# Optimization experiments

Measured on AMD Instinct MI355X. Metric: run time of the kernel, lower is better.

The kernel has to match this reference:

```python
import jax, jax.numpy as jnp
import numpy as np

B, C, H, W = 32, 3, 128, 128
HID, NP, P, E, NH = 64, 64, 16, 768, 4
MAX_SCALE = 0.3


def conv3x3(x, w, b):
    y = jax.lax.conv_general_dilated(x, w, (1, 1), 'SAME', dimension_numbers=('NCHW', 'OIHW', 'NCHW'))
    return y + b[None, :, None, None]


def mha(t, qkv_w, qkv_b, out_w, out_b):
    # t: (B, T, E) -> standard multi-head self-attention (eval: no dropout)
    b, T, e = t.shape
    dh = e // NH
    qkv = t @ qkv_w.T + qkv_b
    q, k, v = jnp.split(qkv, 3, axis=-1)
    sh = lambda z: z.reshape(b, T, NH, dh).transpose(0, 2, 1, 3)
    q, k, v = sh(q), sh(k), sh(v)
    a = jax.nn.softmax(jnp.einsum('bhqd,bhkd->bhqk', q, k) * np.float32(1.0 / np.sqrt(dh)), axis=-1)
    o = jnp.einsum('bhqk,bhkd->bhqd', a, v).transpose(0, 2, 1, 3).reshape(b, T, e)
    return o @ out_w.T + out_b


def conv_self_attn(x, in_w, in_b, qkv_w, qkv_b, out_w, out_b, proj_w, proj_b):
    # channels are tokens; project spatial dim H*W -> E, attend, project back
    b, c, h, w = x.shape
    t = x.reshape(b, c, h * w) @ in_w.T + in_b
    t = mha(t, qkv_w, qkv_b, out_w, out_b)
    y = t @ proj_w.T + proj_b
    return y.reshape(b, c, h, w)


def maxpool2(x):
    return jax.lax.reduce_window(x, -jnp.inf, jax.lax.max, (1, 1, 2, 2), (1, 1, 2, 2), 'VALID')


def grid_sample_bilinear(img, gx, gy):
    # img: (B,C,H,W); gx,gy: (B,NP,P,P) normalized coords; align_corners=False, zeros padding
    b, c, h, w = img.shape
    xs = ((gx + 1.0) * w - 1.0) * 0.5
    ys = ((gy + 1.0) * h - 1.0) * 0.5
    x0f = jnp.floor(xs); y0f = jnp.floor(ys)
    wx = xs - x0f; wy = ys - y0f
    x0 = x0f.astype(jnp.int32); x1 = x0 + 1
    y0 = y0f.astype(jnp.int32); y1 = y0 + 1
    flat = img.reshape(b, c, h * w)

    def gather(yi, xi):
        valid = (xi >= 0) & (xi < w) & (yi >= 0) & (yi < h)
        idx = jnp.clip(yi, 0, h - 1) * w + jnp.clip(xi, 0, w - 1)
        vals = jax.vmap(lambda f, i: f[:, i])(flat, idx)  # (B,C,NP,P,P)
        return vals * valid[:, None].astype(img.dtype)

    v00 = gather(y0, x0); v01 = gather(y0, x1)
    v10 = gather(y1, x0); v11 = gather(y1, x1)
    wxb = wx[:, None]; wyb = wy[:, None]  # (B,1,NP,P,P)
    out = (v00 * (1 - wxb) * (1 - wyb) + v01 * wxb * (1 - wyb)
           + v10 * (1 - wxb) * wyb + v11 * wxb * wyb)
    return out.transpose(0, 2, 1, 3, 4).reshape(b * NP, c, P, P)


def setup_inputs() -> dict:
    key = jax.random.key(0)
    ks = jax.random.split(key, 32)
    wgt = lambda k, s: jax.random.normal(k, s, dtype=jnp.float32) * 0.02
    HW1, HW2, HC = H * W, (H // 2) * (W // 2), (H // 2) * (W // 2)
    inp = {}
    inp['x'] = jax.random.normal(ks[0], (B, C, H, W), dtype=jnp.float32)
    inp['conv1_w'] = wgt(ks[1], (HID, C, 3, 3)); inp['conv1_b'] = jnp.zeros((HID,), jnp.float32)
    inp['a1_in_w'] = wgt(ks[2], (E, HW1)); inp['a1_in_b'] = jnp.zeros((E,), jnp.float32)
    inp['a1_qkv_w'] = wgt(ks[3], (3 * E, E)); inp['a1_qkv_b'] = jnp.zeros((3 * E,), jnp.float32)
    inp['a1_out_w'] = wgt(ks[4], (E, E)); inp['a1_out_b'] = jnp.zeros((E,), jnp.float32)
    inp['a1_proj_w'] = wgt(ks[5], (HW1, E)); inp['a1_proj_b'] = jnp.zeros((HW1,), jnp.float32)
    inp['conv2_w'] = wgt(ks[6], (NP, HID, 3, 3)); inp['conv2_b'] = jnp.zeros((NP,), jnp.float32)
    inp['a2_in_w'] = wgt(ks[7], (E, HW2)); inp['a2_in_b'] = jnp.zeros((E,), jnp.float32)
    inp['a2_qkv_w'] = wgt(ks[8], (3 * E, E)); inp['a2_qkv_b'] = jnp.zeros((3 * E,), jnp.float32)
    inp['a2_out_w'] = wgt(ks[9], (E, E)); inp['a2_out_b'] = jnp.zeros((E,), jnp.float32)
    inp['a2_proj_w'] = wgt(ks[10], (HW2, E)); inp['a2_proj_b'] = jnp.zeros((HW2,), jnp.float32)
    inp['fc1_w'] = wgt(ks[11], (HC // 2, HC)); inp['fc1_b'] = jnp.zeros((HC // 2,), jnp.float32)
    inp['fc2_w'] = wgt(ks[12], (4, HC // 2)); inp['fc2_b'] = jnp.zeros((4,), jnp.float32)
    return inp


def reference(x, conv1_w, conv1_b, a1_in_w, a1_in_b, a1_qkv_w, a1_qkv_b, a1_out_w, a1_out_b,
              a1_proj_w, a1_proj_b, conv2_w, conv2_b, a2_in_w, a2_in_b, a2_qkv_w, a2_qkv_b,
              a2_out_w, a2_out_b, a2_proj_w, a2_proj_b, fc1_w, fc1_b, fc2_w, fc2_b):
    b = x.shape[0]
    f = jax.nn.relu(conv3x3(x, conv1_w, conv1_b))
    f = conv_self_attn(f, a1_in_w, a1_in_b, a1_qkv_w, a1_qkv_b, a1_out_w, a1_out_b, a1_proj_w, a1_proj_b)
    f = maxpool2(f)
    f = jax.nn.relu(conv3x3(f, conv2_w, conv2_b))
    f = conv_self_attn(f, a2_in_w, a2_in_b, a2_qkv_w, a2_qkv_b, a2_out_w, a2_out_b, a2_proj_w, a2_proj_b)
    feats = f.reshape(b, NP, -1)
    h1 = jax.nn.relu(feats @ fc1_w.T + fc1_b)
    tp = h1 @ fc2_w.T + fc2_b  # (b, NP, 4)
    translate = jnp.tanh(tp[:, :, :2])
    s = jax.nn.sigmoid(tp[:, :, 2:3]) * MAX_SCALE
    sx = s[:, :, 0]; sy = s[:, :, 0]  # isotropic: repeat
    rot = jnp.tanh(tp[:, :, 3]) * np.float32(np.pi)
    cos = jnp.cos(rot); sin = jnp.sin(rot)
    x_ext = jnp.minimum(sx * jnp.abs(cos) + sy * jnp.abs(sin), 1.0)
    y_ext = jnp.minimum(sx * jnp.abs(sin) + sy * jnp.abs(cos), 1.0)
    translate = translate * (1.0 - jnp.stack([x_ext, y_ext], axis=-1))
    ta = sx * cos; tb_ = -sx * sin; tc = sy * sin; td = sy * cos
    tx = translate[:, :, 0]; ty = translate[:, :, 1]
    base = (2.0 * jnp.arange(P, dtype=jnp.float32) + 1.0) / P - 1.0  # align_corners=False grid
    gx = ta[..., None, None] * base[None, None, None, :] + tb_[..., None, None] * base[None, None, :, None] + tx[..., None, None]
    gy = tc[..., None, None] * base[None, None, None, :] + td[..., None, None] * base[None, None, :, None] + ty[..., None, None]
    patches = grid_sample_bilinear(x, gx, gy)  # (B*NP, C, P, P)
    return (patches, translate)
```

## Files before the change

kernel.cpp:

```cpp
#include <hip/hip_runtime.h>
#include <hip/hip_bf16.h>
#include <math.h>


#define PI_F 3.14159265358979323846f

typedef float f32x4 __attribute__((ext_vector_type(4)));
typedef short short8 __attribute__((ext_vector_type(8)));
typedef unsigned short us4 __attribute__((ext_vector_type(4)));
typedef __hip_bfloat16 bf16;

__device__ __forceinline__ void async16(const void* g, void* l) {
  __builtin_amdgcn_global_load_lds(
      (const __attribute__((address_space(1))) void*)g,
      (__attribute__((address_space(3))) void*)l, 16, 0, 0);
}

template <int MODE>
__global__ __launch_bounds__(256) void gemm_bf16(
    const unsigned short* __restrict__ A, const unsigned short* __restrict__ Bw,
    const float* __restrict__ bias, void* __restrict__ Cout,
    int M, int N, int K, int kchunk) {
  __shared__ unsigned short As[128 * 32];
  __shared__ unsigned short Bs[128 * 32];
  const int tid = threadIdx.x;
  const int bm = blockIdx.y << 7, bn = blockIdx.x << 7;
  const int k0 = blockIdx.z * kchunk;
  const int wave = tid >> 6;
  const int lane = tid & 63;
  const int wm = (wave & 1) << 6, wn = (wave >> 1) << 6;
  const int r0 = tid >> 2;
  const int c0 = (tid & 3) << 3;
  const unsigned short* Ag0 = A + (size_t)(bm + r0) * K + k0 + c0;
  const unsigned short* Ag1 = Ag0 + (size_t)64 * K;
  const unsigned short* Bg0 = Bw + (size_t)(bn + r0) * K + k0 + c0;
  const unsigned short* Bg1 = Bg0 + (size_t)64 * K;
  unsigned short* Al = As + wave * 512;
  unsigned short* Bl = Bs + wave * 512;
  f32x4 acc[4][4] = {};
  const int fr = lane & 15;
  const int fk = (lane >> 4) << 3;
  for (int kt = 0; kt < kchunk; kt += 32) {
    async16(Ag0 + kt, Al);
    async16(Ag1 + kt, Al + 2048);
    async16(Bg0 + kt, Bl);
    async16(Bg1 + kt, Bl + 2048);
    __syncthreads();
    short8 af[4], bf[4];
    #pragma unroll
    for (int i = 0; i < 4; ++i)
      af[i] = *(const short8*)(As + ((wm + i * 16 + fr) << 5) + fk);
    #pragma unroll
    for (int i = 0; i < 4; ++i)
      bf[i] = *(const short8*)(Bs + ((wn + i * 16 + fr) << 5) + fk);
    #pragma unroll
    for (int mi = 0; mi < 4; ++mi)
      #pragma unroll
      for (int ni = 0; ni < 4; ++ni)
        acc[mi][ni] = __builtin_amdgcn_mfma_f32_16x16x32_bf16(af[mi], bf[ni], acc[mi][ni], 0, 0, 0);
    __syncthreads();
  }
  const int cr = (lane >> 4) << 2;
  const int cc = lane & 15;
  if (MODE == 0) {
    float* C = (float*)Cout + (size_t)blockIdx.z * M * N;
    #pragma unroll
    for (int mi = 0; mi < 4; ++mi)
      #pragma unroll
      for (int ni = 0; ni < 4; ++ni) {
        int col = bn + wn + ni * 16 + cc;
        #pragma unroll
        for (int r = 0; r < 4; ++r)
          C[(size_t)(bm + wm + mi * 16 + cr + r) * N + col] = acc[mi][ni][r];
      }
  } else {
    #pragma unroll
    for (int ni = 0; ni < 4; ++ni) {
      int col = bn + wn + ni * 16 + cc;
      float bv = bias[col];
      #pragma unroll
      for (int mi = 0; mi < 4; ++mi)
        #pragma unroll
        for (int r = 0; r < 4; ++r) {
          size_t idx = (size_t)(bm + wm + mi * 16 + cr + r) * N + col;
          float v = acc[mi][ni][r] + bv;
          if (MODE == 1) ((float*)Cout)[idx] = v;
          else ((bf16*)Cout)[idx] = __float2bfloat16(v);
        }
    }
  }
}

__global__ __launch_bounds__(256) void reduce_bias_k(
    const float* __restrict__ part, const float* __restrict__ bias,
    bf16* __restrict__ out, int MN, int N, int S, int relu) {
  int i = blockIdx.x * 256 + threadIdx.x;
  if (i >= MN) return;
  float s = 0.f;
  for (int z = 0; z < S; ++z) s += part[(size_t)z * MN + i];
  s += bias[i % N];
  if (relu) s = fmaxf(s, 0.f);
  out[i] = __float2bfloat16(s);
}

__global__ __launch_bounds__(256) void cvt_bf16_k(
    const float* __restrict__ src, bf16* __restrict__ dst, int n4) {
  int i = blockIdx.x * 256 + threadIdx.x;
  if (i >= n4) return;
  float4 v = ((const float4*)src)[i];
  bf16* d = dst + (size_t)i * 4;
  d[0] = __float2bfloat16(v.x); d[1] = __float2bfloat16(v.y);
  d[2] = __float2bfloat16(v.z); d[3] = __float2bfloat16(v.w);
}

__global__ __launch_bounds__(256) void cvt_wcl_k(
    const float* __restrict__ w, bf16* __restrict__ wcl) {
  int i = blockIdx.x * 256 + threadIdx.x;
  if (i >= 36864) return;
  int ic = i & 63, oc = (i >> 6) & 63, s = i >> 12;
  wcl[i] = __float2bfloat16(w[oc * 576 + ic * 9 + s]);
}

__global__ __launch_bounds__(256) void conv3x3_relu_c3_fast(
    const float* __restrict__ x, const float* __restrict__ w,
    const float* __restrict__ bias, bf16* __restrict__ out) {
  __shared__ float xs[3][4][132];
  __shared__ float wsm[3][9][64];
  const int tid = threadIdx.x;
  const int b = blockIdx.y;
  const int y0 = blockIdx.x * 2;
  const int xg = (tid & 15) * 8;
  const int row = (tid >> 4) & 1;
  const int oc0 = (tid >> 5) * 8;
  for (int i = tid; i < 3 * 4 * 132; i += 256) {
    int c = i % 132;
    int r = (i / 132) % 4;
    int ic = i / (132 * 4);
    int gy = y0 + r - 1;
    int gx = c - 1;
    float v = 0.f;
    if ((unsigned)gy < 128u && (unsigned)gx < 128u)
      v = x[((size_t)(b * 3 + ic) << 14) + gy * 128 + gx];
    xs[ic][r][c] = v;
  }
  for (int i = tid; i < 3 * 9 * 64; i += 256) {
    int oc = i & 63;
    int k = (i >> 6) % 9;
    int ic = i / (64 * 9);
    wsm[ic][k][oc] = w[oc * 27 + ic * 9 + k];
  }
  __syncthreads();
  float acc[8][8] = {};
  #pragma unroll
  for (int ic = 0; ic < 3; ++ic) {
    #pragma unroll
    for (int ky = 0; ky < 3; ++ky) {
      const float* rp = &xs[ic][row + ky][xg];
      float4 r0 = *(const float4*)(rp);
      float4 r1 = *(const float4*)(rp + 4);
      float4 r2 = *(const float4*)(rp + 8);
      float v[10] = {r0.x, r0.y, r0.z, r0.w, r1.x, r1.y, r1.z, r1.w, r2.x, r2.y};
      #pragma unroll
      for (int kx = 0; kx < 3; ++kx) {
        const float* wr = &wsm[ic][ky * 3 + kx][oc0];
        float4 w0 = *(const float4*)(wr);
        float4 w1 = *(const float4*)(wr + 4);
        float wv[8] = {w0.x, w0.y, w0.z, w0.w, w1.x, w1.y, w1.z, w1.w};
        #pragma unroll
        for (int o = 0; o < 8; ++o)
          #pragma unroll
          for (int p = 0; p < 8; ++p)
            acc[o][p] += wv[o] * v[p + kx];
      }
    }
  }
  #pragma unroll
  for (int o = 0; o < 8; ++o) {
    float bo = bias[oc0 + o];
    bf16 vals[8];
    #pragma unroll
    for (int p = 0; p < 8; ++p) vals[p] = __float2bfloat16(fmaxf(acc[o][p] + bo, 0.f));
    bf16* op = out + ((size_t)(b * 64 + oc0 + o) << 14) + (y0 + row) * 128 + xg;
    *(uint4*)op = *(const uint4*)vals;
  }
}

__global__ __launch_bounds__(256) void maxpool_cl(
    const bf16* __restrict__ y1, bf16* __restrict__ xp) {
  int wave = threadIdx.x >> 6;
  int lane = threadIdx.x & 63;
  int cell = blockIdx.x * 4 + wave;
  int b = blockIdx.y;
  int yp = cell / 66, xq = cell % 66;
  bf16* dst = xp + (((size_t)b * 66 + yp) * 66 + xq) * 64 + lane;
  if (yp == 0 || yp == 65 || xq == 0 || xq == 65) {
    *dst = __float2bfloat16(0.f);
    return;
  }
  int py = yp - 1, px = xq - 1;
  const bf16* sp = y1 + ((size_t)(b * 64 + lane) << 14) + (py * 2) * 128 + px * 2;
  float a = __bfloat162float(sp[0]), bq = __bfloat162float(sp[1]);
  float c = __bfloat162float(sp[128]), d = __bfloat162float(sp[129]);
  *dst = __float2bfloat16(fmaxf(fmaxf(a, bq), fmaxf(c, d)));
}

__global__ __launch_bounds__(256) void conv2_mfma(
    const bf16* __restrict__ xp, const bf16* __restrict__ wcl,
    const float* __restrict__ bias, bf16* __restrict__ f3) {
  __shared__ unsigned short As[128 * 32];
  __shared__ unsigned short Bs[64 * 32];
  const int tid = threadIdx.x;
  const int b = blockIdx.y;
  const int y0 = blockIdx.x * 2;
  const int wave = tid >> 6;
  const int lane = tid & 63;
  const int wm = (wave & 1) << 6;
  const int wn = (wave >> 1) << 5;
  const char* xpB = (const char*)(xp + (size_t)b * 66 * 66 * 64);
  const char* wclB = (const char*)wcl;
  const int sr = tid >> 2;
  const int soff = (tid & 3) << 4;
  unsigned short* Al = As + wave * 512;
  unsigned short* Bl = Bs + wave * 512;
  f32x4 acc[4][2] = {};
  const int fr = lane & 15;
  const int fk = (lane >> 4) << 3;
  for (int tap = 0; tap < 9; ++tap) {
    int dy = tap / 3, dx = tap % 3;
    const char* arow0 = xpB + (((y0 + dy) * 66 + dx) << 7);
    const char* brow = wclB + (tap << 13);
    #pragma unroll
    for (int ch = 0; ch < 2; ++ch) {
      int coff = (ch << 6) + soff;
      async16(arow0 + sr * 128 + coff, Al);
      async16(arow0 + 66 * 128 + sr * 128 + coff, Al + 2048);
      async16(brow + sr * 128 + coff, Bl);
      __syncthreads();
      short8 af[4], bf[2];
      #pragma unroll
      for (int i = 0; i < 4; ++i)
        af[i] = *(const short8*)(As + ((wm + i * 16 + fr) << 5) + fk);
      #pragma unroll
      for (int i = 0; i < 2; ++i)
        bf[i] = *(const short8*)(Bs + ((wn + i * 16 + fr) << 5) + fk);
      #pragma unroll
      for (int mi = 0; mi < 4; ++mi)
        #pragma unroll
        for (int ni = 0; ni < 2; ++ni)
          acc[mi][ni] = __builtin_amdgcn_mfma_f32_16x16x32_bf16(af[mi], bf[ni], acc[mi][ni], 0, 0, 0);
      __syncthreads();
    }
  }
  const int cr = (lane >> 4) << 2;
  const int cc = lane & 15;
  #pragma unroll
  for (int ni = 0; ni < 2; ++ni) {
    int oc = wn + ni * 16 + cc;
    float bv = bias[oc];
    #pragma unroll
    for (int mi = 0; mi < 4; ++mi) {
      int pxb = wm + mi * 16 + cr;
      int y = y0 + (pxb >> 6), xb = pxb & 63;
      bf16 vals[4];
      #pragma unroll
      for (int r = 0; r < 4; ++r)
        vals[r] = __float2bfloat16(fmaxf(acc[mi][ni][r] + bv, 0.f));
      bf16* op = f3 + (((size_t)(b * 64 + oc)) << 12) + y * 64 + xb;
      *(us4*)op = *(const us4*)vals;
    }
  }
}

__global__ __launch_bounds__(64) void attn_scores(
    const float* __restrict__ qkv, float* __restrict__ p, float scale) {
  int tq = blockIdx.x, h = blockIdx.y, b = blockIdx.z;
  int lane = threadIdx.x;
  __shared__ float qrow[192];
  const float* qp = qkv + ((size_t)(b * 64 + tq)) * 2304 + h * 192;
  for (int d = lane; d < 192; d += 64) qrow[d] = qp[d];
  __syncthreads();
  const float* kp = qkv + ((size_t)(b * 64 + lane)) * 2304 + 768 + h * 192;
  float s = 0.f;
  for (int d = 0; d < 192; ++d) s += qrow[d] * kp[d];
  s *= scale;
  float m = s;
  for (int off = 32; off; off >>= 1) m = fmaxf(m, __shfl_xor(m, off));
  float e = expf(s - m);
  float sum = e;
  for (int off = 32; off; off >>= 1) sum += __shfl_xor(sum, off);
  p[(((size_t)b * 4 + h) * 64 + tq) * 64 + lane] = e / sum;
}

__global__ __launch_bounds__(256) void attn_o(
    const float* __restrict__ p, const float* __restrict__ qkv, bf16* __restrict__ o) {
  size_t tid = (size_t)blockIdx.x * 256 + threadIdx.x;
  if (tid >= (size_t)32 * 64 * 768) return;
  int e = (int)(tid % 768);
  int tq = (int)((tid / 768) % 64);
  int b = (int)(tid / (768 * 64));
  int h = e / 192;
  const float* pp = p + (((size_t)b * 4 + h) * 64 + tq) * 64;
  const float* vp = qkv + (size_t)b * 64 * 2304 + 1536 + e;
  float acc = 0.f;
  for (int tk = 0; tk < 64; ++tk) acc += pp[tk] * vp[(size_t)tk * 2304];
  o[tid] = __float2bfloat16(acc);
}

__global__ __launch_bounds__(256) void fc2_wave(
    const bf16* __restrict__ A, const float* __restrict__ Bw,
    const float* __restrict__ bias, float* __restrict__ C, int K) {
  int m = blockIdx.x;
  int n = threadIdx.x >> 6;
  int lane = threadIdx.x & 63;
  const bf16* a = A + (size_t)m * K;
  const float* bb = Bw + (size_t)n * K;
  float acc = 0.f;
  for (int k = lane; k < K; k += 64)
    acc += __bfloat162float(a[k]) * bb[k];
  for (int off = 32; off; off >>= 1) acc += __shfl_xor(acc, off);
  if (lane == 0) C[m * 4 + n] = acc + bias[n];
}

__global__ __launch_bounds__(64) void params_k(
    const float* __restrict__ tp, float* __restrict__ par, float* __restrict__ trans_out) {
  int m = blockIdx.x * 64 + threadIdx.x;
  if (m >= 2048) return;
  float t0 = tp[m * 4 + 0], t1 = tp[m * 4 + 1], t2 = tp[m * 4 + 2], t3 = tp[m * 4 + 3];
  float trx = tanhf(t0), tryy = tanhf(t1);
  float s = (1.f / (1.f + expf(-t2))) * 0.3f;
  float rot = tanhf(t3) * PI_F;
  float c = cosf(rot), sn = sinf(rot);
  float x_ext = fminf(s * fabsf(c) + s * fabsf(sn), 1.f);
  float y_ext = fminf(s * fabsf(sn) + s * fabsf(c), 1.f);
  float tx = trx * (1.f - x_ext);
  float ty = tryy * (1.f - y_ext);
  par[m * 8 + 0] = s * c;
  par[m * 8 + 1] = -s * sn;
  par[m * 8 + 2] = s * sn;
  par[m * 8 + 3] = s * c;
  par[m * 8 + 4] = tx;
  par[m * 8 + 5] = ty;
  trans_out[m * 2 + 0] = tx;
  trans_out[m * 2 + 1] = ty;
}

__global__ __launch_bounds__(256) void sample_k(
    const float* __restrict__ x, const float* __restrict__ par, float* __restrict__ out) {
  int tid = blockIdx.x * 256 + threadIdx.x;
  if (tid >= 32 * 64 * 3 * 256) return;
  int pj = tid & 15, pi = (tid >> 4) & 15;
  int c = (tid >> 8) % 3;
  int bp = tid / 768;
  int b = bp >> 6;
  const float* pp = par + bp * 8;
  float ta = pp[0], tb = pp[1], tc = pp[2], td = pp[3], tx = pp[4], ty = pp[5];
  float bj = (2.f * pj + 1.f) / 16.f - 1.f;
  float bi = (2.f * pi + 1.f) / 16.f - 1.f;
  float gx = ta * bj + tb * bi + tx;
  float gy = tc * bj + td * bi + ty;
  float xs = ((gx + 1.f) * 128.f - 1.f) * 0.5f;
  float ys = ((gy + 1.f) * 128.f - 1.f) * 0.5f;
  float x0f = floorf(xs), y0f = floorf(ys);
  float wx = xs - x0f, wy = ys - y0f;
  int x0 = (int)x0f, y0 = (int)y0f, x1 = x0 + 1, y1 = y0 + 1;
  const float* img = x + ((size_t)b * 3 + c) * 16384;
  auto g = [&](int yi, int xi) -> float {
    bool v = (xi >= 0) && (xi < 128) && (yi >= 0) && (yi < 128);
    int yc = yi < 0 ? 0 : (yi > 127 ? 127 : yi);
    int xc = xi < 0 ? 0 : (xi > 127 ? 127 : xi);
    float val = img[yc * 128 + xc];
    return v ? val : 0.f;
  };
  float v00 = g(y0, x0), v01 = g(y0, x1), v10 = g(y1, x0), v11 = g(y1, x1);
  out[tid] = v00 * (1.f - wx) * (1.f - wy) + v01 * wx * (1.f - wy) +
             v10 * (1.f - wx) * wy + v11 * wx * wy;
}

static inline void cvt(const float* src, bf16* dst, int n, hipStream_t s) {
  int n4 = n / 4;
  cvt_bf16_k<<<(n4 + 255) / 256, 256, 0, s>>>(src, dst, n4);
}

extern "C" void kernel_launch(void* const* d_in, const int* in_sizes, int n_in,
                              void* d_out, int out_size, void* d_ws, size_t ws_size,
                              hipStream_t stream) {
  const float* x        = (const float*)d_in[0];
  const float* conv1_w  = (const float*)d_in[1];
  const float* conv1_b  = (const float*)d_in[2];
  const float* a1_in_w  = (const float*)d_in[3];
  const float* a1_in_b  = (const float*)d_in[4];
  const float* a1_qkv_w = (const float*)d_in[5];
  const float* a1_qkv_b = (const float*)d_in[6];
  const float* a1_out_w = (const float*)d_in[7];
  const float* a1_out_b = (const float*)d_in[8];
  const float* a1_proj_w = (const float*)d_in[9];
  const float* a1_proj_b = (const float*)d_in[10];
  const float* conv2_w  = (const float*)d_in[11];
  const float* conv2_b  = (const float*)d_in[12];
  const float* a2_in_w  = (const float*)d_in[13];
  const float* a2_in_b  = (const float*)d_in[14];
  const float* a2_qkv_w = (const float*)d_in[15];
  const float* a2_qkv_b = (const float*)d_in[16];
  const float* a2_out_w = (const float*)d_in[17];
  const float* a2_out_b = (const float*)d_in[18];
  const float* a2_proj_w = (const float*)d_in[19];
  const float* a2_proj_b = (const float*)d_in[20];
  const float* fc1_w    = (const float*)d_in[21];
  const float* fc1_b    = (const float*)d_in[22];
  const float* fc2_w    = (const float*)d_in[23];
  const float* fc2_b    = (const float*)d_in[24];
  float* out = (float*)d_out;

  char* ws = (char*)d_ws;
  bf16*  f1   = (bf16*)(ws + 0);
  bf16*  y1   = f1;
  bf16*  f3   = (bf16*)(ws + 0);
  bf16*  h1   = (bf16*)(ws + 33554432);
  float* part = (float*)(ws + 83886080);
  bf16*  xp   = (bf16*)(ws + 83886080);
  bf16*  t    = (bf16*)(ws + 134217728);
  float* qkv  = (float*)(ws + 137363456);
  float* p    = (float*)(ws + 156237824);
  bf16*  o    = (bf16*)(ws + 158334976);
  bf16*  ao   = (bf16*)(ws + 161480704);
  bf16*  y2   = (bf16*)(ws + 164626432);
  float* tp   = (float*)(ws + 181403648);
  float* par  = (float*)(ws + 181436416);
  bf16*  W    = (bf16*)(ws + 181501952);
  bf16*  wcl  = W;

  const unsigned short* Wu = (const unsigned short*)W;
  const float scale = 0.07216878364870323f;

  conv3x3_relu_c3_fast<<<dim3(64, 32), 256, 0, stream>>>(x, conv1_w, conv1_b, f1);
  cvt(a1_in_w, W, 768 * 16384, stream);
  gemm_bf16<0><<<dim3(6, 16, 8), 256, 0, stream>>>((const unsigned short*)f1, Wu, nullptr, part, 2048, 768, 16384, 2048);
  reduce_bias_k<<<6144, 256, 0, stream>>>(part, a1_in_b, t, 2048 * 768, 768, 8, 0);
  cvt(a1_qkv_w, W, 2304 * 768, stream);
  gemm_bf16<1><<<dim3(18, 16, 1), 256, 0, stream>>>((const unsigned short*)t, Wu, a1_qkv_b, qkv, 2048, 2304, 768, 768);
  attn_scores<<<dim3(64, 4, 32), 64, 0, stream>>>(qkv, p, scale);
  attn_o<<<6144, 256, 0, stream>>>(p, qkv, o);
  cvt(a1_out_w, W, 768 * 768, stream);
  gemm_bf16<0><<<dim3(6, 16, 3), 256, 0, stream>>>((const unsigned short*)o, Wu, nullptr, part, 2048, 768, 768, 256);
  reduce_bias_k<<<6144, 256, 0, stream>>>(part, a1_out_b, ao, 2048 * 768, 768, 3, 0);
  cvt(a1_proj_w, W, 16384 * 768, stream);
  gemm_bf16<2><<<dim3(128, 16, 1), 256, 0, stream>>>((const unsigned short*)ao, Wu, a1_proj_b, y1, 2048, 16384, 768, 768);
  cvt_wcl_k<<<144, 256, 0, stream>>>(conv2_w, wcl);
  maxpool_cl<<<dim3(1089, 32), 256, 0, stream>>>(y1, xp);
  conv2_mfma<<<dim3(32, 32), 256, 0, stream>>>(xp, wcl, conv2_b, f3);
  cvt(a2_in_w, W, 768 * 4096, stream);
  gemm_bf16<0><<<dim3(6, 16, 4), 256, 0, stream>>>((const unsigned short*)f3, Wu, nullptr, part, 2048, 768, 4096, 1024);
  reduce_bias_k<<<6144, 256, 0, stream>>>(part, a2_in_b, t, 2048 * 768, 768, 4, 0);
  cvt(a2_qkv_w, W, 2304 * 768, stream);
  gemm_bf16<1><<<dim3(18, 16, 1), 256, 0, stream>>>((const unsigned short*)t, Wu, a2_qkv_b, qkv, 2048, 2304, 768, 768);
  attn_scores<<<dim3(64, 4, 32), 64, 0, stream>>>(qkv, p, scale);
  attn_o<<<6144, 256, 0, stream>>>(p, qkv, o);
  cvt(a2_out_w, W, 768 * 768, stream);
  gemm_bf16<0><<<dim3(6, 16, 3), 256, 0, stream>>>((const unsigned short*)o, Wu, nullptr, part, 2048, 768, 768, 256);
  reduce_bias_k<<<6144, 256, 0, stream>>>(part, a2_out_b, ao, 2048 * 768, 768, 3, 0);
  cvt(a2_proj_w, W, 4096 * 768, stream);
  gemm_bf16<2><<<dim3(32, 16, 1), 256, 0, stream>>>((const unsigned short*)ao, Wu, a2_proj_b, y2, 2048, 4096, 768, 768);
  cvt(fc1_w, W, 2048 * 4096, stream);
  gemm_bf16<0><<<dim3(16, 16, 2), 256, 0, stream>>>((const unsigned short*)y2, Wu, nullptr, part, 2048, 2048, 4096, 2048);
  reduce_bias_k<<<16384, 256, 0, stream>>>(part, fc1_b, h1, 2048 * 2048, 2048, 2, 1);
  fc2_wave<<<2048, 256, 0, stream>>>(h1, fc2_w, fc2_b, tp, 2048);
  params_k<<<32, 64, 0, stream>>>(tp, par, out + 1572864);
  sample_k<<<6144, 256, 0, stream>>>(x, par, out);
}
```

Baseline: 941.0 us.

## Swizzle GEMM tile order, vectorize split-K reduce, batch weight conversions

Replaces the 2D GEMM grid with a 1D grid remapped into groups of 8 M-tiles so that neighbouring blocks share B tiles and A rows in L2. The split-K reduction now processes float4 and writes four bf16 values at a time. The in/qkv/out weight conversions for each attention block are merged into one kernel writing to separate buffers, which removes launches. Placing Wq/Wo in the y2 region relies on those regions not being live at the same time.

```diff
diff --git a/kernel.cpp b/kernel.cpp
--- a/kernel.cpp
+++ b/kernel.cpp
@@ -24,7 +24,15 @@
   __shared__ unsigned short As[128 * 32];
   __shared__ unsigned short Bs[128 * 32];
   const int tid = threadIdx.x;
-  const int bm = blockIdx.y << 7, bn = blockIdx.x << 7;
+  const int bmT = M >> 7, bnT = N >> 7;
+  int l = blockIdx.x;
+  const int gsize = 8 * bnT;
+  int gid = l / gsize;
+  int rem = l - gid * gsize;
+  int fm = gid * 8;
+  int gsz = bmT - fm; if (gsz > 8) gsz = 8;
+  const int bm = (fm + rem % gsz) << 7;
+  const int bn = (rem / gsz) << 7;
   const int k0 = blockIdx.z * kchunk;
   const int wave = tid >> 6;
   const int lane = tid & 63;
@@ -95,22 +103,40 @@
     const float* __restrict__ part, const float* __restrict__ bias,
     bf16* __restrict__ out, int MN, int N, int S, int relu) {
   int i = blockIdx.x * 256 + threadIdx.x;
-  if (i >= MN) return;
-  float s = 0.f;
-  for (int z = 0; z < S; ++z) s += part[(size_t)z * MN + i];
-  s += bias[i % N];
-  if (relu) s = fmaxf(s, 0.f);
-  out[i] = __float2bfloat16(s);
-}
-
-__global__ __launch_bounds__(256) void cvt_bf16_k(
-    const float* __restrict__ src, bf16* __restrict__ dst, int n4) {
+  if (i >= (MN >> 2)) return;
+  float4 s = ((const float4*)part)[i];
+  for (int z = 1; z < S; ++z) {
+    float4 q = *(const float4*)(part + (size_t)z * MN + i * 4);
+    s.x += q.x; s.y += q.y; s.z += q.z; s.w += q.w;
+  }
+  int nb = (i * 4) % N;
+  float4 bv = *(const float4*)(bias + nb);
+  s.x += bv.x; s.y += bv.y; s.z += bv.z; s.w += bv.w;
+  if (relu) {
+    s.x = fmaxf(s.x, 0.f); s.y = fmaxf(s.y, 0.f);
+    s.z = fmaxf(s.z, 0.f); s.w = fmaxf(s.w, 0.f);
+  }
+  bf16 vals[4] = {__float2bfloat16(s.x), __float2bfloat16(s.y),
+                  __float2bfloat16(s.z), __float2bfloat16(s.w)};
+  *(us4*)(out + (size_t)i * 4) = *(const us4*)vals;
+}
+
+__global__ __launch_bounds__(256) void cvt3_k(
+    const float* __restrict__ s0, bf16* __restrict__ d0, int n0,
+    const float* __restrict__ s1, bf16* __restrict__ d1, int n1,
+    const float* __restrict__ s2, bf16* __restrict__ d2, int n2) {
   int i = blockIdx.x * 256 + threadIdx.x;
-  if (i >= n4) return;
-  float4 v = ((const float4*)src)[i];
-  bf16* d = dst + (size_t)i * 4;
-  d[0] = __float2bfloat16(v.x); d[1] = __float2bfloat16(v.y);
-  d[2] = __float2bfloat16(v.z); d[3] = __float2bfloat16(v.w);
+  const float* s; bf16* d; int j = i;
+  if (j < n0) { s = s0; d = d0; }
+  else {
+    j -= n0;
+    if (j < n1) { s = s1; d = d1; }
+    else { j -= n1; if (j >= n2) return; s = s2; d = d2; }
+  }
+  float4 v = ((const float4*)s)[j];
+  bf16 vals[4] = {__float2bfloat16(v.x), __float2bfloat16(v.y),
+                  __float2bfloat16(v.z), __float2bfloat16(v.w)};
+  *(us4*)(d + (size_t)j * 4) = *(const us4*)vals;
 }
 
 __global__ __launch_bounds__(256) void cvt_wcl_k(
@@ -376,11 +402,6 @@
              v10 * (1.f - wx) * wy + v11 * wx * wy;
 }
 
-static inline void cvt(const float* src, bf16* dst, int n, hipStream_t s) {
-  int n4 = n / 4;
-  cvt_bf16_k<<<(n4 + 255) / 256, 256, 0, s>>>(src, dst, n4);
-}
-
 extern "C" void kernel_launch(void* const* d_in, const int* in_sizes, int n_in,
                               void* d_out, int out_size, void* d_ws, size_t ws_size,
                               hipStream_t stream) {
@@ -428,41 +449,50 @@
   float* par  = (float*)(ws + 181436416);
   bf16*  W    = (bf16*)(ws + 181501952);
   bf16*  wcl  = W;
+  bf16*  Wq   = (bf16*)(ws + 164626432);
+  bf16*  Wo   = (bf16*)(ws + 164626432 + 3538944);
 
   const unsigned short* Wu = (const unsigned short*)W;
+  const unsigned short* Wqu = (const unsigned short*)Wq;
+  const unsigned short* Wou = (const unsigned short*)Wo;
   const float scale = 0.07216878364870323f;
 
+  const int n_in1 = 768 * 16384 / 4, n_qkv = 2304 * 768 / 4, n_out = 768 * 768 / 4;
+  const int n_in2 = 768 * 4096 / 4;
+  const int n_proj1 = 16384 * 768 / 4, n_proj2 = 4096 * 768 / 4, n_fc1 = 2048 * 4096 / 4;
+
   conv3x3_relu_c3_fast<<<dim3(64, 32), 256, 0, stream>>>(x, conv1_w, conv1_b, f1);
-  cvt(a1_in_w, W, 768 * 16384, stream);
-  gemm_bf16<0><<<dim3(6, 16, 8), 256, 0, stream>>>((const unsigned short*)f1, Wu, nullptr, part, 2048, 768, 16384, 2048);
-  reduce_bias_k<<<6144, 256, 0, stream>>>(part, a1_in_b, t, 2048 * 768, 768, 8, 0);
-  cvt(a1_qkv_w, W, 2304 * 768, stream);
-  gemm_bf16<1><<<dim3(18, 16, 1), 256, 0, stream>>>((const unsigned short*)t, Wu, a1_qkv_b, qkv, 2048, 2304, 768, 768);
+  cvt3_k<<<(n_in1 + n_qkv + n_out + 255) / 256, 256, 0, stream>>>(
+      a1_in_w, W, n_in1, a1_qkv_w, Wq, n_qkv, a1_out_w, Wo, n_out);
+  gemm_bf16<0><<<dim3(96, 1, 8), 256, 0, stream>>>((const unsigned short*)f1, Wu, nullptr, part, 2048, 768, 16384, 2048);
+  reduce_bias_k<<<1536, 256, 0, stream>>>(part, a1_in_b, t, 2048 * 768, 768, 8, 0);
+  gemm_bf16<1><<<dim3(288, 1, 1), 256, 0, stream>>>((const unsigned short*)t, Wqu, a1_qkv_b, qkv, 2048, 2304, 768, 768);
   attn_scores<<<dim3(64, 4, 32), 64, 0, stream>>>(qkv, p, scale);
   attn_o<<<6144, 256, 0, stream>>>(p, qkv, o);
-  cvt(a1_out_w, W, 768 * 768, stream);
-  gemm_bf16<0><<<dim3(6, 16, 3), 256, 0, stream>>>((const unsigned short*)o, Wu, nullptr, part, 2048, 768, 768, 256);
-  reduce_bias_k<<<6144, 256, 0, stream>>>(part, a1_out_b, ao, 2048 * 768, 768, 3, 0);
-  cvt(a1_proj_w, W, 16384 * 768, stream);
-  gemm_bf16<2><<<dim3(128, 16, 1), 256, 0, stream>>>((const unsigned short*)ao, Wu, a1_proj_b, y1, 2048, 16384, 768, 768);
+  gemm_bf16<0><<<dim3(96, 1, 3), 256, 0, stream>>>((const unsigned short*)o, Wou, nullptr, part, 2048, 768, 768, 256);
+  reduce_bias_k<<<1536, 256, 0, stream>>>(part, a1_out_b, ao, 2048 * 768, 768, 3, 0);
+  cvt3_k<<<(n_proj1 + 255) / 256, 256, 0, stream>>>(
+      a1_proj_w, W, n_proj1, nullptr, nullptr, 0, nullptr, nullptr, 0);
+  gemm_bf16<2><<<dim3(2048, 1, 1), 256, 0, stream>>>((const unsigned short*)ao, Wu, a1_proj_b, y1, 2048, 16384, 768, 768);
   cvt_wcl_k<<<144, 256, 0, stream>>>(conv2_w, wcl);
   maxpool_cl<<<dim3(1089, 32), 256, 0, stream>>>(y1, xp);
   conv2_mfma<<<dim3(32, 32), 256, 0, stream>>>(xp, wcl, conv2_b, f3);
-  cvt(a2_in_w, W, 768 * 4096, stream);
-  gemm_bf16<0><<<dim3(6, 16, 4), 256, 0, stream>>>((const unsigned short*)f3, Wu, nullptr, part, 2048, 768, 4096, 1024);
-  reduce_bias_k<<<6144, 256, 0, stream>>>(part, a2_in_b, t, 2048 * 768, 768, 4, 0);
-  cvt(a2_qkv_w, W, 2304 * 768, stream);
-  gemm_bf16<1><<<dim3(18, 16, 1), 256, 0, stream>>>((const unsigned short*)t, Wu, a2_qkv_b, qkv, 2048, 2304, 768, 768);
+  cvt3_k<<<(n_in2 + n_qkv + n_out + 255) / 256, 256, 0, stream>>>(
+      a2_in_w, W, n_in2, a2_qkv_w, Wq, n_qkv, a2_out_w, Wo, n_out);
+  gemm_bf16<0><<<dim3(96, 1, 4), 256, 0, stream>>>((const unsigned short*)f3, Wu, nullptr, part, 2048, 768, 4096, 1024);
+  reduce_bias_k<<<1536, 256, 0, stream>>>(part, a2_in_b, t, 2048 * 768, 768, 4, 0);
+  gemm_bf16<1><<<dim3(288, 1, 1), 256, 0, stream>>>((const unsigned short*)t, Wqu, a2_qkv_b, qkv, 2048, 2304, 768, 768);
   attn_scores<<<dim3(64, 4, 32), 64, 0, stream>>>(qkv, p, scale);
   attn_o<<<6144, 256, 0, stream>>>(p, qkv, o);
-  cvt(a2_out_w, W, 768 * 768, stream);
-  gemm_bf16<0><<<dim3(6, 16, 3), 256, 0, stream>>>((const unsigned short*)o, Wu, nullptr, part, 2048, 768, 768, 256);
-  reduce_bias_k<<<6144, 256, 0, stream>>>(part, a2_out_b, ao, 2048 * 768, 768, 3, 0);
-  cvt(a2_proj_w, W, 4096 * 768, stream);
-  gemm_bf16<2><<<dim3(32, 16, 1), 256, 0, stream>>>((const unsigned short*)ao, Wu, a2_proj_b, y2, 2048, 4096, 768, 768);
-  cvt(fc1_w, W, 2048 * 4096, stream);
-  gemm_bf16<0><<<dim3(16, 16, 2), 256, 0, stream>>>((const unsigned short*)y2, Wu, nullptr, part, 2048, 2048, 4096, 2048);
-  reduce_bias_k<<<16384, 256, 0, stream>>>(part, fc1_b, h1, 2048 * 2048, 2048, 2, 1);
+  gemm_bf16<0><<<dim3(96, 1, 3), 256, 0, stream>>>((const unsigned short*)o, Wou, nullptr, part, 2048, 768, 768, 256);
+  reduce_bias_k<<<1536, 256, 0, stream>>>(part, a2_out_b, ao, 2048 * 768, 768, 3, 0);
+  cvt3_k<<<(n_proj2 + 255) / 256, 256, 0, stream>>>(
+      a2_proj_w, W, n_proj2, nullptr, nullptr, 0, nullptr, nullptr, 0);
+  gemm_bf16<2><<<dim3(512, 1, 1), 256, 0, stream>>>((const unsigned short*)ao, Wu, a2_proj_b, y2, 2048, 4096, 768, 768);
+  cvt3_k<<<(n_fc1 + 255) / 256, 256, 0, stream>>>(
+      fc1_w, W, n_fc1, nullptr, nullptr, 0, nullptr, nullptr, 0);
+  gemm_bf16<0><<<dim3(256, 1, 2), 256, 0, stream>>>((const unsigned short*)y2, Wu, nullptr, part, 2048, 2048, 4096, 2048);
+  reduce_bias_k<<<4096, 256, 0, stream>>>(part, fc1_b, h1, 2048 * 2048, 2048, 2, 1);
   fc2_wave<<<2048, 256, 0, stream>>>(h1, fc2_w, fc2_b, tp, 2048);
   params_k<<<32, 64, 0, stream>>>(tp, par, out + 1572864);
   sample_k<<<6144, 256, 0, stream>>>(x, par, out);
```

After: 902.3 us. 4.1% less time.
